# Kernel optimization log

Measured on AMD Instinct MI355X. Metric: run time of the kernel, lower is better.

The kernel has to match this reference:

```python
import jax, jax.numpy as jnp
import numpy as np

N = 50000        # nodes
E = 1_600_000    # edges (avg degree 32)
D_IN = 128       # node_input_dim
EMB = 32         # node_input_dim // 4
H = 256          # hidden dim (all 3 layers)
OUT = 128        # output_dim
L = 3            # num gnn layers
B = 8            # graphs in batch
NUM_TYPES = 3
LN_EPS = 1e-5


def setup_inputs() -> dict:
    key = jax.random.key(0)
    ks = jax.random.split(key, 14)
    x = jax.random.normal(ks[0], (N, D_IN), dtype=jnp.float32)
    edge_index = jax.random.randint(ks[1], (2, E), 0, N)
    node_types = jax.random.randint(ks[2], (N,), 0, NUM_TYPES)
    batch = jnp.sort(jax.random.randint(ks[3], (N,), 0, B))
    s = lambda fan_in: 1.0 / np.sqrt(fan_in)
    emb = jax.random.normal(ks[4], (NUM_TYPES, EMB), dtype=jnp.float32)
    W_in = jax.random.normal(ks[5], (D_IN + EMB, H), dtype=jnp.float32) * s(D_IN + EMB)
    b_in = jnp.zeros((H,), dtype=jnp.float32)
    Ws = jax.random.normal(ks[6], (L, H, H), dtype=jnp.float32) * s(H)
    bs = jnp.zeros((L, H), dtype=jnp.float32)
    gammas = jnp.ones((L, H), dtype=jnp.float32)
    betas = jnp.zeros((L, H), dtype=jnp.float32)
    W_out = jax.random.normal(ks[7], (H, OUT), dtype=jnp.float32) * s(H)
    b_out = jnp.zeros((OUT,), dtype=jnp.float32)
    return {"x": x, "edge_index": edge_index, "node_types": node_types,
            "batch": batch, "emb": emb, "W_in": W_in, "b_in": b_in,
            "Ws": Ws, "bs": bs, "gammas": gammas, "betas": betas,
            "W_out": W_out, "b_out": b_out}


def _layer_norm(h, g, b):
    mu = jnp.mean(h, axis=-1, keepdims=True)
    var = jnp.mean((h - mu) ** 2, axis=-1, keepdims=True)
    return (h - mu) * jax.lax.rsqrt(var + LN_EPS) * g + b


def _gcn_conv(h, src, dst, W, b):
    # GCNConv: X W, then sym-normalized aggregation with self-loops, then bias.
    m = h @ W                                   # [N, H]
    loops = jnp.arange(N)
    s_idx = jnp.concatenate([src, loops])
    d_idx = jnp.concatenate([dst, loops])
    deg = jax.ops.segment_sum(jnp.ones(E + N, h.dtype), d_idx, num_segments=N)
    dinv = jnp.where(deg > 0, jax.lax.rsqrt(deg), 0.0)
    norm = dinv[s_idx] * dinv[d_idx]            # [E+N]
    out = jax.ops.segment_sum(m[s_idx] * norm[:, None], d_idx, num_segments=N)
    return out + b


def reference(x, edge_index, node_types, batch, emb, W_in, b_in,
              Ws, bs, gammas, betas, W_out, b_out):
    src, dst = edge_index[0], edge_index[1]
    # node type embedding + concat + input projection + relu
    h = jnp.concatenate([x, emb[node_types]], axis=-1)
    h = jax.nn.relu(h @ W_in + b_in)
    # GNN layers: conv -> layernorm -> relu -> residual (dropout is eval no-op)
    for l in range(L):
        residual = h
        h = _gcn_conv(h, src, dst, Ws[l], bs[l])
        h = jax.nn.relu(_layer_norm(h, gammas[l], betas[l]))
        h = h + residual
    node_features = h @ W_out + b_out           # [N, OUT]
    # global mean pool by graph index
    sums = jax.ops.segment_sum(node_features, batch, num_segments=B)
    cnts = jax.ops.segment_sum(jnp.ones((N,), node_features.dtype), batch, num_segments=B)
    return sums / jnp.maximum(cnts, 1.0)[:, None]   # [B, OUT]
```

## Files before the change

### kernel.cpp

```cpp
#include <hip/hip_runtime.h>
#include <math.h>

#define HID 256
#define DXIN 128
#define EMBD 32
#define OUTD 128
#define NLAYER 3
#define NGRAPH 8
#define LN_EPS 1e-5f
#define BKP 264
#define NBLK 256

typedef short s8v __attribute__((ext_vector_type(8)));
typedef float f4v __attribute__((ext_vector_type(4)));
typedef float f2v __attribute__((ext_vector_type(2)));

__device__ __forceinline__ float b2f_lo(unsigned int u) {
  return __builtin_bit_cast(float, u << 16);
}
__device__ __forceinline__ float b2f_hi(unsigned int u) {
  return __builtin_bit_cast(float, u & 0xffff0000u);
}
__device__ __forceinline__ unsigned short f2b(float f) {
  unsigned int x = __builtin_bit_cast(unsigned int, f);
  unsigned int lsb = (x >> 16) & 1u;
  x += 0x7fffu + lsb;
  return (unsigned short)(x >> 16);
}

__global__ __launch_bounds__(256) void k_b1(const int* __restrict__ dst,
                                            int* __restrict__ blk_cnt, int E, int epb) {
  __shared__ int hist[256];
  int blk = blockIdx.x, tid = threadIdx.x;
  hist[tid] = 0;
  __syncthreads();
  int beg = blk * epb, end = min(E, beg + epb);
  for (int i = beg + tid; i < end; i += 256)
    atomicAdd(&hist[dst[i] >> 8], 1);
  __syncthreads();
  blk_cnt[blk * 256 + tid] = hist[tid];
}

__global__ __launch_bounds__(256) void k_bsum(const int* __restrict__ blk_cnt,
                                              int* __restrict__ bucket_cnt) {
  __shared__ int red[4];
  int b = blockIdx.x, tid = threadIdx.x;
  int v = blk_cnt[tid * 256 + b];
#pragma unroll
  for (int o = 32; o > 0; o >>= 1) v += __shfl_xor(v, o, 64);
  if ((tid & 63) == 0) red[tid >> 6] = v;
  __syncthreads();
  if (tid == 0) bucket_cnt[b] = red[0] + red[1] + red[2] + red[3];
}

__global__ __launch_bounds__(256) void k_bscan(const int* __restrict__ bucket_cnt,
                                               int* __restrict__ bucket_base,
                                               int* __restrict__ row_ptr,
                                               int N, int nbuck, int E) {
  __shared__ int s[256];
  int tid = threadIdx.x;
  int v = (tid < nbuck) ? bucket_cnt[tid] : 0;
  s[tid] = v;
  __syncthreads();
  for (int off = 1; off < 256; off <<= 1) {
    int t = (tid >= off) ? s[tid - off] : 0;
    __syncthreads();
    s[tid] += t;
    __syncthreads();
  }
  if (tid < nbuck) bucket_base[tid] = s[tid] - v;
  if (tid == 0) { bucket_base[nbuck] = E; row_ptr[N] = E; }
}

__global__ __launch_bounds__(256) void k_boff(const int* __restrict__ blk_cnt,
                                              const int* __restrict__ bucket_base,
                                              int* __restrict__ blk_off) {
  __shared__ int s[256];
  int b = blockIdx.x, tid = threadIdx.x;
  int v = blk_cnt[tid * 256 + b];
  s[tid] = v;
  __syncthreads();
  for (int off = 1; off < 256; off <<= 1) {
    int t = (tid >= off) ? s[tid - off] : 0;
    __syncthreads();
    s[tid] += t;
    __syncthreads();
  }
  blk_off[tid * 256 + b] = bucket_base[b] + s[tid] - v;
}

__global__ __launch_bounds__(256) void k_b3(const int* __restrict__ ei,
                                            const int* __restrict__ blk_off,
                                            unsigned int* __restrict__ pairs,
                                            int E, int epb) {
  __shared__ int cur[256];
  int blk = blockIdx.x, tid = threadIdx.x;
  cur[tid] = blk_off[blk * 256 + tid];
  __syncthreads();
  int beg = blk * epb, end = min(E, beg + epb);
  for (int i = beg + tid; i < end; i += 256) {
    int s = ei[i];
    int d = ei[E + i];
    int pos = atomicAdd(&cur[d >> 8], 1);
    pairs[pos] = (unsigned int)s | ((unsigned int)(d & 255) << 16);
  }
}

__global__ __launch_bounds__(256) void k_b4(const unsigned int* __restrict__ pairs,
                                            const int* __restrict__ bucket_base,
                                            int* __restrict__ row_ptr,
                                            float* __restrict__ dinv,
                                            int* __restrict__ col_idx, int N) {
  __shared__ int cnt[256];
  __shared__ int s[256];
  int b = blockIdx.x, tid = threadIdx.x;
  int base = bucket_base[b], end = bucket_base[b + 1];
  cnt[tid] = 0;
  __syncthreads();
  for (int i = base + tid; i < end; i += 256)
    atomicAdd(&cnt[pairs[i] >> 16], 1);
  __syncthreads();
  int c = cnt[tid];
  s[tid] = c;
  __syncthreads();
  for (int off = 1; off < 256; off <<= 1) {
    int t = (tid >= off) ? s[tid - off] : 0;
    __syncthreads();
    s[tid] += t;
    __syncthreads();
  }
  int excl = s[tid] - c;
  int d = (b << 8) + tid;
  if (d < N) {
    row_ptr[d] = base + excl;
    dinv[d] = rsqrtf((float)(c + 1));
  }
  __syncthreads();
  cnt[tid] = base + excl;
  __syncthreads();
  for (int i = base + tid; i < end; i += 256) {
    unsigned int w = pairs[i];
    int pos = atomicAdd(&cnt[w >> 16], 1);
    col_idx[pos] = (int)(w & 0xFFFFu);
  }
}

__global__ void k_pack(const float* __restrict__ W, unsigned short* __restrict__ dst,
                       int C, int NKS, int total) {
  int t = blockIdx.x * 256 + threadIdx.x;
  if (t >= total) return;
  int j = t & 7;
  int l = (t >> 3) & 63;
  int rest = t >> 9;
  int ks = rest % NKS;
  int ct = rest / NKS;
  int k = ks * 32 + ((l >> 4) << 3) + j;
  int c = ct * 16 + (l & 15);
  dst[t] = f2b(W[(size_t)k * C + c]);
}

__global__ __launch_bounds__(256) void k_mfma_in(
    const float* __restrict__ x, const int* __restrict__ nt, const float* __restrict__ emb,
    const unsigned short* __restrict__ Wpk, const float* __restrict__ bias,
    unsigned short* __restrict__ h, int N) {
  __shared__ unsigned short a_lds[64 * BKP];
  int tid = threadIdx.x;
  int w = tid >> 6, l = tid & 63;
  int row0 = blockIdx.x * 64;

  for (int i = 0; i < 4; ++i) {
    int cc = i * 256 + tid;
    int r = cc >> 4, ch = cc & 15;
    int row = row0 + r;
    unsigned short tmp[8];
    if (row < N) {
      const float* xr = &x[(size_t)row * DXIN + ch * 8];
      float4 v0 = *(const float4*)xr;
      float4 v1 = *(const float4*)(xr + 4);
      tmp[0] = f2b(v0.x); tmp[1] = f2b(v0.y); tmp[2] = f2b(v0.z); tmp[3] = f2b(v0.w);
      tmp[4] = f2b(v1.x); tmp[5] = f2b(v1.y); tmp[6] = f2b(v1.z); tmp[7] = f2b(v1.w);
    } else {
      for (int q = 0; q < 8; ++q) tmp[q] = 0;
    }
    *(uint4*)&a_lds[r * BKP + ch * 8] = *(const uint4*)tmp;
  }
  {
    int r = tid >> 2, ch = tid & 3;
    int row = row0 + r;
    unsigned short tmp[8];
    if (row < N) {
      int typ = nt[row];
      const float* er = &emb[typ * EMBD + ch * 8];
      float4 v0 = *(const float4*)er;
      float4 v1 = *(const float4*)(er + 4);
      tmp[0] = f2b(v0.x); tmp[1] = f2b(v0.y); tmp[2] = f2b(v0.z); tmp[3] = f2b(v0.w);
      tmp[4] = f2b(v1.x); tmp[5] = f2b(v1.y); tmp[6] = f2b(v1.z); tmp[7] = f2b(v1.w);
    } else {
      for (int q = 0; q < 8; ++q) tmp[q] = 0;
    }
    *(uint4*)&a_lds[r * BKP + DXIN + ch * 8] = *(const uint4*)tmp;
  }
  __syncthreads();

  f4v acc[4][4];
#pragma unroll
  for (int rt = 0; rt < 4; ++rt)
#pragma unroll
    for (int ct = 0; ct < 4; ++ct) acc[rt][ct] = (f4v)0.f;

  for (int ks = 0; ks < 5; ++ks) {
    s8v af[4];
#pragma unroll
    for (int rt = 0; rt < 4; ++rt)
      af[rt] = *(const s8v*)&a_lds[(rt * 16 + (l & 15)) * BKP + ks * 32 + (l >> 4) * 8];
#pragma unroll
    for (int ct = 0; ct < 4; ++ct) {
      s8v bf = *(const s8v*)&Wpk[(size_t)(((w * 4 + ct) * 5 + ks) * 64 + l) * 8];
#pragma unroll
      for (int rt = 0; rt < 4; ++rt)
        acc[rt][ct] = __builtin_amdgcn_mfma_f32_16x16x32_bf16(af[rt], bf, acc[rt][ct], 0, 0, 0);
    }
  }
  __syncthreads();

#pragma unroll
  for (int rt = 0; rt < 4; ++rt)
#pragma unroll
    for (int ct = 0; ct < 4; ++ct) {
      int col = w * 64 + ct * 16 + (l & 15);
      float bv = bias[col];
#pragma unroll
      for (int reg = 0; reg < 4; ++reg) {
        int r = rt * 16 + (l >> 4) * 4 + reg;
        a_lds[r * BKP + col] = f2b(fmaxf(acc[rt][ct][reg] + bv, 0.f));
      }
    }
  __syncthreads();
  for (int i = 0; i < 8; ++i) {
    int cc = i * 256 + tid;
    int r = cc >> 5, ch = cc & 31;
    int row = row0 + r;
    if (row < N)
      *(uint4*)&h[(size_t)row * HID + ch * 8] = *(const uint4*)&a_lds[r * BKP + ch * 8];
  }
}

__global__ __launch_bounds__(256) void k_mfma_sq(
    const unsigned short* __restrict__ A, const unsigned short* __restrict__ Wpk,
    unsigned char* __restrict__ m8, int N) {
  __shared__ unsigned short a_lds[64 * BKP];
  int tid = threadIdx.x;
  int w = tid >> 6, l = tid & 63;
  int row0 = blockIdx.x * 64;

  for (int i = 0; i < 8; ++i) {
    int cc = i * 256 + tid;
    int r = cc >> 5, ch = cc & 31;
    int row = row0 + r;
    uint4 v = make_uint4(0u, 0u, 0u, 0u);
    if (row < N) v = *(const uint4*)&A[(size_t)row * HID + ch * 8];
    *(uint4*)&a_lds[r * BKP + ch * 8] = v;
  }
  __syncthreads();

  f4v acc[4][4];
#pragma unroll
  for (int rt = 0; rt < 4; ++rt)
#pragma unroll
    for (int ct = 0; ct < 4; ++ct) acc[rt][ct] = (f4v)0.f;

  for (int ks = 0; ks < 8; ++ks) {
    s8v af[4];
#pragma unroll
    for (int rt = 0; rt < 4; ++rt)
      af[rt] = *(const s8v*)&a_lds[(rt * 16 + (l & 15)) * BKP + ks * 32 + (l >> 4) * 8];
#pragma unroll
    for (int ct = 0; ct < 4; ++ct) {
      s8v bf = *(const s8v*)&Wpk[(size_t)(((w * 4 + ct) * 8 + ks) * 64 + l) * 8];
#pragma unroll
      for (int rt = 0; rt < 4; ++rt)
        acc[rt][ct] = __builtin_amdgcn_mfma_f32_16x16x32_bf16(af[rt], bf, acc[rt][ct], 0, 0, 0);
    }
  }
  __syncthreads();

#pragma unroll
  for (int rt = 0; rt < 4; ++rt)
#pragma unroll
    for (int ct = 0; ct < 4; ++ct) {
      int col = w * 64 + ct * 16 + (l & 15);
#pragma unroll
      for (int reg = 0; reg < 4; ++reg) {
        int r = rt * 16 + (l >> 4) * 4 + reg;
        a_lds[r * BKP + col] = f2b(acc[rt][ct][reg]);
      }
    }
  __syncthreads();
  for (int i = 0; i < 8; ++i) {
    int cc = i * 256 + tid;
    int r = cc >> 5, ch = cc & 31;
    int row = row0 + r;
    if (row < N) {
      uint4 v = *(const uint4*)&a_lds[r * BKP + ch * 8];
      float f0 = b2f_lo(v.x), f1 = b2f_hi(v.x);
      float f2 = b2f_lo(v.y), f3 = b2f_hi(v.y);
      float f4 = b2f_lo(v.z), f5 = b2f_hi(v.z);
      float f6 = b2f_lo(v.w), f7 = b2f_hi(v.w);
      unsigned int p0 = 0, p1 = 0;
      p0 = __builtin_amdgcn_cvt_pk_fp8_f32(f0, f1, p0, 0);
      p0 = __builtin_amdgcn_cvt_pk_fp8_f32(f2, f3, p0, 1);
      p1 = __builtin_amdgcn_cvt_pk_fp8_f32(f4, f5, p1, 0);
      p1 = __builtin_amdgcn_cvt_pk_fp8_f32(f6, f7, p1, 1);
      *(uint2*)&m8[(size_t)row * HID + ch * 8] = make_uint2(p0, p1);
    }
  }
}

__global__ __launch_bounds__(256) void k_mfma_out_pool(
    const unsigned short* __restrict__ A, const unsigned short* __restrict__ Wpk,
    const float* __restrict__ bias, const int* __restrict__ batch,
    float* __restrict__ psum, int N) {
  __shared__ unsigned short a_lds[64 * BKP];
  __shared__ float pool[NGRAPH * OUTD];
  __shared__ int b_s[64];
  int tid = threadIdx.x;
  int w = tid >> 6, l = tid & 63;
  int row0 = blockIdx.x * 64;

#pragma unroll
  for (int i = 0; i < 4; ++i) pool[tid * 4 + i] = 0.f;
  if (tid < 64) b_s[tid] = (row0 + tid < N) ? batch[row0 + tid] : -1;

  for (int i = 0; i < 8; ++i) {
    int cc = i * 256 + tid;
    int r = cc >> 5, ch = cc & 31;
    int row = row0 + r;
    uint4 v = make_uint4(0u, 0u, 0u, 0u);
    if (row < N) v = *(const uint4*)&A[(size_t)row * HID + ch * 8];
    *(uint4*)&a_lds[r * BKP + ch * 8] = v;
  }
  __syncthreads();

  f4v acc[4][2];
#pragma unroll
  for (int rt = 0; rt < 4; ++rt)
#pragma unroll
    for (int ct = 0; ct < 2; ++ct) acc[rt][ct] = (f4v)0.f;

  for (int ks = 0; ks < 8; ++ks) {
    s8v af[4];
#pragma unroll
    for (int rt = 0; rt < 4; ++rt)
      af[rt] = *(const s8v*)&a_lds[(rt * 16 + (l & 15)) * BKP + ks * 32 + (l >> 4) * 8];
#pragma unroll
    for (int ct = 0; ct < 2; ++ct) {
      s8v bf = *(const s8v*)&Wpk[(size_t)(((w * 2 + ct) * 8 + ks) * 64 + l) * 8];
#pragma unroll
      for (int rt = 0; rt < 4; ++rt)
        acc[rt][ct] = __builtin_amdgcn_mfma_f32_16x16x32_bf16(af[rt], bf, acc[rt][ct], 0, 0, 0);
    }
  }

#pragma unroll
  for (int ct = 0; ct < 2; ++ct) {
    int col = w * 32 + ct * 16 + (l & 15);
    float bv = bias[col];
    float run = 0.f;
    int cur = -1;
#pragma unroll
    for (int rt = 0; rt < 4; ++rt)
#pragma unroll
      for (int reg = 0; reg < 4; ++reg) {
        int rrel = rt * 16 + (l >> 4) * 4 + reg;
        int g = b_s[rrel];
        if (g != cur) {
          if (cur >= 0) atomicAdd(&pool[cur * OUTD + col], run);
          run = 0.f;
          cur = g;
        }
        if (g >= 0) run += acc[rt][ct][reg] + bv;
      }
    if (cur >= 0) atomicAdd(&pool[cur * OUTD + col], run);
  }
  __syncthreads();
#pragma unroll
  for (int i = 0; i < 4; ++i) {
    int idx = tid * 4 + i;
    float v = pool[idx];
    if (v != 0.f) atomicAdd(&psum[idx], v);
  }
}

__global__ __launch_bounds__(256) void k_agg_ln(
    const unsigned char* __restrict__ m8, unsigned short* __restrict__ h,
    const int* __restrict__ row_ptr, const int* __restrict__ col_idx,
    const float* __restrict__ dinv, const float* __restrict__ bias,
    const float* __restrict__ gamma, const float* __restrict__ beta, int N) {
  int w = threadIdx.x >> 6, l = threadIdx.x & 63;
  int d = blockIdx.x * 4 + w;
  if (d >= N) return;
  int c0 = l * 4;
  float dv = dinv[d];

  unsigned int sv = *(const unsigned int*)&m8[((size_t)d << 8) + c0];
  f2v slo = __builtin_amdgcn_cvt_pk_f32_fp8(sv, 0);
  f2v shi = __builtin_amdgcn_cvt_pk_f32_fp8(sv, 1);
  float a0 = slo[0] * dv;
  float a1 = slo[1] * dv;
  float a2 = shi[0] * dv;
  float a3 = shi[1] * dv;

  int beg = row_ptr[d], end = row_ptr[d + 1];
#pragma unroll 4
  for (int jj = beg; jj < end; ++jj) {
    int s = col_idx[jj];
    float ws = dinv[s];
    unsigned int v = *(const unsigned int*)&m8[((size_t)s << 8) + c0];
    f2v lo = __builtin_amdgcn_cvt_pk_f32_fp8(v, 0);
    f2v hi = __builtin_amdgcn_cvt_pk_f32_fp8(v, 1);
    a0 += ws * lo[0];
    a1 += ws * lo[1];
    a2 += ws * hi[0];
    a3 += ws * hi[1];
  }

  float4 bv = *(const float4*)&bias[c0];
  a0 = a0 * dv + bv.x;
  a1 = a1 * dv + bv.y;
  a2 = a2 * dv + bv.z;
  a3 = a3 * dv + bv.w;

  float t = a0 + a1 + a2 + a3;
#pragma unroll
  for (int o = 32; o > 0; o >>= 1) t += __shfl_xor(t, o, 64);
  float mu = t * (1.f / 256.f);
  float d0 = a0 - mu, d1 = a1 - mu, d2 = a2 - mu, d3 = a3 - mu;
  float v2 = d0 * d0 + d1 * d1 + d2 * d2 + d3 * d3;
#pragma unroll
  for (int o = 32; o > 0; o >>= 1) v2 += __shfl_xor(v2, o, 64);
  float rs = rsqrtf(v2 * (1.f / 256.f) + LN_EPS);

  float4 gv = *(const float4*)&gamma[c0];
  float4 bt = *(const float4*)&beta[c0];
  uint2 hv = *(const uint2*)&h[(size_t)d * HID + c0];
  float y0 = fmaxf(d0 * rs * gv.x + bt.x, 0.f) + b2f_lo(hv.x);
  float y1 = fmaxf(d1 * rs * gv.y + bt.y, 0.f) + b2f_hi(hv.x);
  float y2 = fmaxf(d2 * rs * gv.z + bt.z, 0.f) + b2f_lo(hv.y);
  float y3 = fmaxf(d3 * rs * gv.w + bt.w, 0.f) + b2f_hi(hv.y);
  uint2 ov;
  ov.x = (unsigned int)f2b(y0) | ((unsigned int)f2b(y1) << 16);
  ov.y = (unsigned int)f2b(y2) | ((unsigned int)f2b(y3) << 16);
  *(uint2*)&h[(size_t)d * HID + c0] = ov;
}

__global__ void k_final(const float* __restrict__ psum, const int* __restrict__ batch,
                        float* __restrict__ out, int N) {
  int t = threadIdx.x;
  int b = t >> 7;
  int lo = 0, hi = N;
  while (lo < hi) { int mid = (lo + hi) >> 1; if (batch[mid] < b) lo = mid + 1; else hi = mid; }
  int lb = lo;
  lo = 0; hi = N;
  while (lo < hi) { int mid = (lo + hi) >> 1; if (batch[mid] <= b) lo = mid + 1; else hi = mid; }
  int cnt = lo - lb;
  out[t] = psum[t] / fmaxf((float)cnt, 1.f);
}

extern "C" void kernel_launch(void* const* d_in, const int* in_sizes, int n_in,
                              void* d_out, int out_size, void* d_ws, size_t ws_size,
                              hipStream_t stream) {
  const float* x      = (const float*)d_in[0];
  const int*   ei     = (const int*)d_in[1];
  const int*   nt     = (const int*)d_in[2];
  const int*   batch  = (const int*)d_in[3];
  const float* emb    = (const float*)d_in[4];
  const float* W_in   = (const float*)d_in[5];
  const float* b_in   = (const float*)d_in[6];
  const float* Ws     = (const float*)d_in[7];
  const float* bs     = (const float*)d_in[8];
  const float* gammas = (const float*)d_in[9];
  const float* betas  = (const float*)d_in[10];
  const float* W_out  = (const float*)d_in[11];
  const float* b_out  = (const float*)d_in[12];
  float* out = (float*)d_out;

  const int N = in_sizes[2];
  const int E = in_sizes[1] / 2;
  const int nbuck = (N + 255) >> 8;
  const int epb = (E + NBLK - 1) / NBLK;

  auto align = [](size_t v) { return (v + 255) & ~(size_t)255; };
  char* p = (char*)d_ws;
  unsigned short* h = (unsigned short*)p; p += align((size_t)N * HID * 2);
  unsigned char* m8 = (unsigned char*)p;  p += align((size_t)N * HID);
  unsigned short* pk_in  = (unsigned short*)p; p += align(16 * 5 * 512 * 2);
  unsigned short* pk_sq  = (unsigned short*)p; p += align((size_t)3 * 16 * 8 * 512 * 2);
  unsigned short* pk_out = (unsigned short*)p; p += align(8 * 8 * 512 * 2);
  float* dinv = (float*)p;        p += align((size_t)N * 4);
  int* row_ptr = (int*)p;         p += align((size_t)(N + 1) * 4);
  int* col_idx = (int*)p;         p += align((size_t)E * 4);
  unsigned int* pairs = (unsigned int*)p; p += align((size_t)E * 4);
  int* blk_cnt = (int*)p;         p += align((size_t)NBLK * 256 * 4);
  int* blk_off = (int*)p;         p += align((size_t)NBLK * 256 * 4);
  int* bucket_cnt = (int*)p;      p += align(256 * 4);
  int* bucket_base = (int*)p;     p += align(257 * 4);
  float* psum = (float*)p;        p += align((size_t)NGRAPH * OUTD * 4);

  hipMemsetAsync(psum, 0, (size_t)NGRAPH * OUTD * 4, stream);

  {
    int t_in = 16 * 5 * 512;
    k_pack<<<(t_in + 255) / 256, 256, 0, stream>>>(W_in, pk_in, HID, 5, t_in);
    int t_sq = 16 * 8 * 512;
    for (int lyr = 0; lyr < NLAYER; ++lyr)
      k_pack<<<(t_sq + 255) / 256, 256, 0, stream>>>(Ws + (size_t)lyr * HID * HID,
                                                     pk_sq + (size_t)lyr * t_sq, HID, 8, t_sq);
    int t_out = 8 * 8 * 512;
    k_pack<<<(t_out + 255) / 256, 256, 0, stream>>>(W_out, pk_out, OUTD, 8, t_out);
  }

  k_b1<<<NBLK, 256, 0, stream>>>(ei + E, blk_cnt, E, epb);
  k_bsum<<<nbuck, 256, 0, stream>>>(blk_cnt, bucket_cnt);
  k_bscan<<<1, 256, 0, stream>>>(bucket_cnt, bucket_base, row_ptr, N, nbuck, E);
  k_boff<<<nbuck, 256, 0, stream>>>(blk_cnt, bucket_base, blk_off);
  k_b3<<<NBLK, 256, 0, stream>>>(ei, blk_off, pairs, E, epb);
  k_b4<<<nbuck, 256, 0, stream>>>(pairs, bucket_base, row_ptr, dinv, col_idx, N);

  const int GB = (N + 63) / 64;
  k_mfma_in<<<GB, 256, 0, stream>>>(x, nt, emb, pk_in, b_in, h, N);

  for (int lyr = 0; lyr < NLAYER; ++lyr) {
    k_mfma_sq<<<GB, 256, 0, stream>>>(h, pk_sq + (size_t)lyr * 16 * 8 * 512, m8, N);
    k_agg_ln<<<(N + 3) / 4, 256, 0, stream>>>(m8, h, row_ptr, col_idx, dinv,
                                              bs + (size_t)lyr * HID, gammas + (size_t)lyr * HID,
                                              betas + (size_t)lyr * HID, N);
  }

  k_mfma_out_pool<<<GB, 256, 0, stream>>>(h, pk_out, b_out, batch, psum, N);
  k_final<<<1, 1024, 0, stream>>>(psum, batch, out, N);
}
```

Measured before the change: 392.2 us.

## Fold source-side dinv into GEMM epilogue, batch gather loads, merge pack kernels

The source-node normalization dinv[s] is now applied in the k_mfma_sq epilogue before FP8 quantization. This removes the per-edge dinv gather and multiply from the aggregation loop. The gather loop is restructured to issue eight independent neighbor loads before accumulating, to raise memory-level parallelism. The five weight-pack launches are merged into one kernel. Scaling before FP8 conversion slightly changes quantization error.

```diff
diff --git a/kernel.cpp b/kernel.cpp
--- a/kernel.cpp
+++ b/kernel.cpp
@@ -145,10 +145,31 @@
   }
 }
 
-__global__ void k_pack(const float* __restrict__ W, unsigned short* __restrict__ dst,
-                       int C, int NKS, int total) {
+#define T_IN  (16 * 5 * 512)
+#define T_SQ  (16 * 8 * 512)
+#define T_OUT (8 * 8 * 512)
+__global__ void k_pack_all(const float* __restrict__ W_in, const float* __restrict__ Ws,
+                           const float* __restrict__ W_out,
+                           unsigned short* __restrict__ pk_in,
+                           unsigned short* __restrict__ pk_sq,
+                           unsigned short* __restrict__ pk_out) {
   int t = blockIdx.x * 256 + threadIdx.x;
-  if (t >= total) return;
+  const float* W;
+  unsigned short* dst;
+  int C, NKS;
+  if (t < T_IN) {
+    W = W_in; dst = pk_in; C = HID; NKS = 5;
+  } else if (t < T_IN + 3 * T_SQ) {
+    int tt = t - T_IN;
+    int lyr = tt / T_SQ;
+    t = tt - lyr * T_SQ;
+    W = Ws + (size_t)lyr * HID * HID; dst = pk_sq + (size_t)lyr * T_SQ; C = HID; NKS = 8;
+  } else if (t < T_IN + 3 * T_SQ + T_OUT) {
+    t = t - T_IN - 3 * T_SQ;
+    W = W_out; dst = pk_out; C = OUTD; NKS = 8;
+  } else {
+    return;
+  }
   int j = t & 7;
   int l = (t >> 3) & 63;
   int rest = t >> 9;
@@ -247,7 +268,7 @@
 
 __global__ __launch_bounds__(256) void k_mfma_sq(
     const unsigned short* __restrict__ A, const unsigned short* __restrict__ Wpk,
-    unsigned char* __restrict__ m8, int N) {
+    const float* __restrict__ dinv, unsigned char* __restrict__ m8, int N) {
   __shared__ unsigned short a_lds[64 * BKP];
   int tid = threadIdx.x;
   int w = tid >> 6, l = tid & 63;
@@ -301,11 +322,12 @@
     int r = cc >> 5, ch = cc & 31;
     int row = row0 + r;
     if (row < N) {
+      float dv = dinv[row];
       uint4 v = *(const uint4*)&a_lds[r * BKP + ch * 8];
-      float f0 = b2f_lo(v.x), f1 = b2f_hi(v.x);
-      float f2 = b2f_lo(v.y), f3 = b2f_hi(v.y);
-      float f4 = b2f_lo(v.z), f5 = b2f_hi(v.z);
-      float f6 = b2f_lo(v.w), f7 = b2f_hi(v.w);
+      float f0 = b2f_lo(v.x) * dv, f1 = b2f_hi(v.x) * dv;
+      float f2 = b2f_lo(v.y) * dv, f3 = b2f_hi(v.y) * dv;
+      float f4 = b2f_lo(v.z) * dv, f5 = b2f_hi(v.z) * dv;
+      float f6 = b2f_lo(v.w) * dv, f7 = b2f_hi(v.w) * dv;
       unsigned int p0 = 0, p1 = 0;
       p0 = __builtin_amdgcn_cvt_pk_fp8_f32(f0, f1, p0, 0);
       p0 = __builtin_amdgcn_cvt_pk_fp8_f32(f2, f3, p0, 1);
@@ -405,23 +427,39 @@
   unsigned int sv = *(const unsigned int*)&m8[((size_t)d << 8) + c0];
   f2v slo = __builtin_amdgcn_cvt_pk_f32_fp8(sv, 0);
   f2v shi = __builtin_amdgcn_cvt_pk_f32_fp8(sv, 1);
-  float a0 = slo[0] * dv;
-  float a1 = slo[1] * dv;
-  float a2 = shi[0] * dv;
-  float a3 = shi[1] * dv;
+  float a0 = slo[0];
+  float a1 = slo[1];
+  float a2 = shi[0];
+  float a3 = shi[1];
 
   int beg = row_ptr[d], end = row_ptr[d + 1];
-#pragma unroll 4
-  for (int jj = beg; jj < end; ++jj) {
+  int jj = beg;
+  for (; jj + 8 <= end; jj += 8) {
+    unsigned int vv[8];
+#pragma unroll
+    for (int q = 0; q < 8; ++q) {
+      int s = col_idx[jj + q];
+      vv[q] = *(const unsigned int*)&m8[((size_t)s << 8) + c0];
+    }
+#pragma unroll
+    for (int q = 0; q < 8; ++q) {
+      f2v lo = __builtin_amdgcn_cvt_pk_f32_fp8(vv[q], 0);
+      f2v hi = __builtin_amdgcn_cvt_pk_f32_fp8(vv[q], 1);
+      a0 += lo[0];
+      a1 += lo[1];
+      a2 += hi[0];
+      a3 += hi[1];
+    }
+  }
+  for (; jj < end; ++jj) {
     int s = col_idx[jj];
-    float ws = dinv[s];
     unsigned int v = *(const unsigned int*)&m8[((size_t)s << 8) + c0];
     f2v lo = __builtin_amdgcn_cvt_pk_f32_fp8(v, 0);
     f2v hi = __builtin_amdgcn_cvt_pk_f32_fp8(v, 1);
-    a0 += ws * lo[0];
-    a1 += ws * lo[1];
-    a2 += ws * hi[0];
-    a3 += ws * hi[1];
+    a0 += lo[0];
+    a1 += lo[1];
+    a2 += hi[0];
+    a3 += hi[1];
   }
 
   float4 bv = *(const float4*)&bias[c0];
@@ -493,9 +531,9 @@
   char* p = (char*)d_ws;
   unsigned short* h = (unsigned short*)p; p += align((size_t)N * HID * 2);
   unsigned char* m8 = (unsigned char*)p;  p += align((size_t)N * HID);
-  unsigned short* pk_in  = (unsigned short*)p; p += align(16 * 5 * 512 * 2);
-  unsigned short* pk_sq  = (unsigned short*)p; p += align((size_t)3 * 16 * 8 * 512 * 2);
-  unsigned short* pk_out = (unsigned short*)p; p += align(8 * 8 * 512 * 2);
+  unsigned short* pk_in  = (unsigned short*)p; p += align((size_t)T_IN * 2);
+  unsigned short* pk_sq  = (unsigned short*)p; p += align((size_t)3 * T_SQ * 2);
+  unsigned short* pk_out = (unsigned short*)p; p += align((size_t)T_OUT * 2);
   float* dinv = (float*)p;        p += align((size_t)N * 4);
   int* row_ptr = (int*)p;         p += align((size_t)(N + 1) * 4);
   int* col_idx = (int*)p;         p += align((size_t)E * 4);
@@ -509,14 +547,9 @@
   hipMemsetAsync(psum, 0, (size_t)NGRAPH * OUTD * 4, stream);
 
   {
-    int t_in = 16 * 5 * 512;
-    k_pack<<<(t_in + 255) / 256, 256, 0, stream>>>(W_in, pk_in, HID, 5, t_in);
-    int t_sq = 16 * 8 * 512;
-    for (int lyr = 0; lyr < NLAYER; ++lyr)
-      k_pack<<<(t_sq + 255) / 256, 256, 0, stream>>>(Ws + (size_t)lyr * HID * HID,
-                                                     pk_sq + (size_t)lyr * t_sq, HID, 8, t_sq);
-    int t_out = 8 * 8 * 512;
-    k_pack<<<(t_out + 255) / 256, 256, 0, stream>>>(W_out, pk_out, OUTD, 8, t_out);
+    int total = T_IN + 3 * T_SQ + T_OUT;
+    k_pack_all<<<(total + 255) / 256, 256, 0, stream>>>(W_in, Ws, W_out,
+                                                        pk_in, pk_sq, pk_out);
   }
 
   k_b1<<<NBLK, 256, 0, stream>>>(ei + E, blk_cnt, E, epb);
@@ -530,7 +563,7 @@
   k_mfma_in<<<GB, 256, 0, stream>>>(x, nt, emb, pk_in, b_in, h, N);
 
   for (int lyr = 0; lyr < NLAYER; ++lyr) {
-    k_mfma_sq<<<GB, 256, 0, stream>>>(h, pk_sq + (size_t)lyr * 16 * 8 * 512, m8, N);
+    k_mfma_sq<<<GB, 256, 0, stream>>>(h, pk_sq + (size_t)lyr * T_SQ, dinv, m8, N);
     k_agg_ln<<<(N + 3) / 4, 256, 0, stream>>>(m8, h, row_ptr, col_idx, dinv,
                                               bs + (size_t)lyr * HID, gammas + (size_t)lyr * HID,
                                               betas + (size_t)lyr * HID, N);
```

After: 369.2 us. 5.9% less time.
